# Performance work log

Measured on AMD Instinct MI355X. Metric: run time of the kernel, lower is better.

The kernel has to match this reference:

```python
import jax, jax.numpy as jnp
import numpy as np
from jax.scipy.linalg import expm

B = 524288      # batch of states (original module is per-vector; vmapped via batched matmuls)
IN = 64         # input_size
KDIM = 128      # koopman_size
W_PHI = (IN + KDIM) // 2   # 96, encoder MLP hidden width
W_INV = (KDIM + IN) // 2   # 96, decoder MLP hidden width


def setup_inputs() -> dict:
    key = jax.random.key(0)
    ks = jax.random.split(key, 8)
    def w(k, shape, fan_in):
        return jax.random.normal(k, shape, jnp.float32) / np.float32(np.sqrt(fan_in))
    return {
        "t": jnp.asarray(6.0, jnp.float32),                       # hours; module uses t/24
        "x": jax.random.normal(ks[0], (B, IN), jnp.float32),
        "A": jax.random.normal(ks[1], (KDIM, KDIM), jnp.float32) / np.float32(np.sqrt(KDIM)),
        "phi_W1": w(ks[2], (W_PHI, IN), IN),
        "phi_b1": jnp.zeros((W_PHI,), jnp.float32),
        "phi_W2": w(ks[3], (KDIM, W_PHI), W_PHI),                 # no final bias (skip=True)
        "inv_W1": w(ks[4], (W_INV, KDIM), KDIM),
        "inv_b1": jnp.zeros((W_INV,), jnp.float32),
        "inv_W2": w(ks[5], (IN, W_INV), W_INV),
        "inv_b2": jnp.zeros((IN,), jnp.float32),                  # use_final_bias=True (skip=False)
    }


def reference(t, x, A, phi_W1, phi_b1, phi_W2, inv_W1, inv_b1, inv_W2, inv_b2):
    # phi: z = C @ x + MLP(x), C = eye(KDIM, IN) -> zero-pad x into koopman space
    h = jax.nn.relu(x @ phi_W1.T + phi_b1)                # [B, W_PHI]
    z = jnp.pad(x, ((0, 0), (0, KDIM - IN))) + h @ phi_W2.T   # [B, KDIM]
    # Koopman propagation: K = expm(A * t/24); z <- K @ z (batched as z @ K.T)
    Kmat = expm(A * (t / 24.0), max_squarings=20)          # [KDIM, KDIM]
    z = z @ Kmat.T
    # phi_inv: plain MLP with final bias, no skip
    h2 = jax.nn.relu(z @ inv_W1.T + inv_b1)                # [B, W_INV]
    return h2 @ inv_W2.T + inv_b2                          # [B, IN]
```

## Files before the change

### kernel.cpp

```cpp
#include <hip/hip_runtime.h>

#define BTOT    524288
#define NT64    8192
#define GRID    512
#define TN      6

typedef __attribute__((ext_vector_type(8))) short s8v;
typedef __attribute__((ext_vector_type(4))) float f4v;

#define MFMA(a,b,c) __builtin_amdgcn_mfma_f32_16x16x32_bf16((a),(b),(c),0,0,0)
#define KEEP(x) asm volatile("" : "+v"(x))

__device__ __forceinline__ short f2b(float f) {
  union { float f; unsigned u; } v; v.f = f;
  unsigned r = v.u + 0x7fffu + ((v.u >> 16) & 1u);
  return (short)(r >> 16);
}
__device__ __forceinline__ float b2f(short s) {
  union { float f; unsigned u; } v; v.u = ((unsigned)(unsigned short)s) << 16;
  return v.f;
}
__device__ __forceinline__ s8v pack8(f4v u, f4v v) {
  s8v w;
  w[0] = f2b(u[0]); w[1] = f2b(u[1]); w[2] = f2b(u[2]); w[3] = f2b(u[3]);
  w[4] = f2b(v[0]); w[5] = f2b(v[1]); w[6] = f2b(v[2]); w[7] = f2b(v[3]);
  return w;
}

__device__ __forceinline__ s8v ldfrag(const short* base, int row0, int kbase, int stride) {
  const int l = threadIdx.x & 63;
  return *(const s8v*)(base + (row0 + (l & 15)) * stride + kbase + (l >> 4) * 8);
}

#define WS_M1   0
#define WS_I1   8192
#define WS_W1   20480
#define WS_W2K  26624
#define WS_I2   38912

__device__ __forceinline__ int fragidx(int n, int k, int KS) {
  int jj = n >> 4, ks = k >> 5;
  int l = (n & 15) | (((k >> 3) & 3) << 4);
  return ((jj * KS + ks) * 64 + l) * 8 + (k & 7);
}

__global__ __launch_bounds__(512, 2) void koop_prep(
    const float* __restrict__ tptr, const float* __restrict__ Ag,
    const float* __restrict__ W2g, const float* __restrict__ w1g,
    const float* __restrict__ i1g, const float* __restrict__ i2g,
    short* __restrict__ wsp) {
  extern __shared__ __align__(16) char smem[];
  short* RThi = (short*)smem;
  short* RTlo = RThi + 128 * 136;
  float* sW2  = (float*)(RTlo + 128 * 136);
  float* sred = sW2 + 128 * 96;
  float* scratch = (float*)smem;

  const int tid = threadIdx.x;
  const int lane = tid & 63, wid = tid >> 6;
  const int c_ = lane & 15, g_ = lane >> 4;
  const int mr = wid * 16;

  for (int e = tid; e < 6144; e += 512) {
    wsp[WS_W1 + fragidx(e >> 6, e & 63, 2)] = f2b(w1g[e]);
  }
  for (int e = tid; e < 12288; e += 512) {
    wsp[WS_I1 + fragidx(e >> 7, e & 127, 4)] = f2b(i1g[e]);
  }
  for (int e = tid; e < 6144; e += 512) {
    wsp[WS_I2 + fragidx(e / 96, e % 96, 3)] = f2b(i2g[e]);
  }

  const float s = tptr[0] * (1.0f / 24.0f);
  for (int i = tid; i < 128 * 128; i += 512) scratch[i] = Ag[i] * s;
  for (int i = tid; i < 128 * 96;  i += 512) sW2[i] = W2g[i];
  __syncthreads();

  if (tid < 128) {
    float su = 0.f;
    for (int j = 0; j < 128; ++j) su += fabsf(scratch[tid * 128 + j]);
    sred[tid] = su;
  }
  __syncthreads();
  if (tid == 0) {
    float m = 0.f;
    for (int i = 0; i < 128; ++i) m = fmaxf(m, sred[i]);
    int j = 0; float sc = 1.f;
    while (m > 0.5f && j < 20) { m *= 0.5f; sc *= 0.5f; ++j; }
    sred[128] = (float)j; sred[129] = sc;
  }
  __syncthreads();
  const int jsq = (int)sred[128];
  const float sc = sred[129];

  s8v Ahi[4], Alo[4];
#pragma unroll
  for (int ks = 0; ks < 4; ++ks) {
    const float* p = scratch + (mr + c_) * 128 + ks * 32 + g_ * 8;
    f4v u = *(const f4v*)p, v = *(const f4v*)(p + 4);
    float vals[8] = {u[0], u[1], u[2], u[3], v[0], v[1], v[2], v[3]};
#pragma unroll
    for (int i = 0; i < 8; ++i) {
      float y = vals[i] * sc;
      short h = f2b(y);
      Ahi[ks][i] = h;
      Alo[ks][i] = f2b(y - b2f(h));
    }
  }
  float yv[32];
#pragma unroll
  for (int e = 0; e < 32; ++e) yv[e] = scratch[tid * 32 + e];
  __syncthreads();

#pragma unroll
  for (int e = 0; e < 32; ++e) {
    int idx = tid * 32 + e;
    int r = idx >> 7, c = idx & 127;
    float v = yv[e] * sc * (1.0f / TN) + ((r == c) ? 1.0f : 0.0f);
    short h = f2b(v);
    RThi[c * 136 + r] = h;
    RTlo[c * 136 + r] = f2b(v - b2f(h));
  }
  __syncthreads();

  for (int k = TN - 1; k >= 1; --k) {
    f4v acc[8];
#pragma unroll
    for (int nt = 0; nt < 8; ++nt) acc[nt] = (f4v){0.f, 0.f, 0.f, 0.f};
#pragma unroll
    for (int ks = 0; ks < 4; ++ks) {
#pragma unroll
      for (int nt = 0; nt < 8; ++nt) {
        s8v bh = ldfrag(RThi, nt * 16, ks * 32, 136);
        s8v bl = ldfrag(RTlo, nt * 16, ks * 32, 136);
        acc[nt] = MFMA(Ahi[ks], bh, acc[nt]);
        acc[nt] = MFMA(Alo[ks], bh, acc[nt]);
        acc[nt] = MFMA(Ahi[ks], bl, acc[nt]);
      }
    }
    __syncthreads();
    const float invk = 1.0f / (float)k;
#pragma unroll
    for (int nt = 0; nt < 8; ++nt)
#pragma unroll
      for (int r = 0; r < 4; ++r) {
        int row = mr + g_ * 4 + r, col = nt * 16 + c_;
        float v = acc[nt][r] * invk + ((row == col) ? 1.0f : 0.0f);
        short h = f2b(v);
        RThi[col * 136 + row] = h;
        RTlo[col * 136 + row] = f2b(v - b2f(h));
      }
    __syncthreads();
  }

  for (int it = 0; it < jsq; ++it) {
    s8v Shi[4], Slo[4];
#pragma unroll
    for (int ks = 0; ks < 4; ++ks) {
      int m = mr + c_;
      int k0 = ks * 32 + g_ * 8;
#pragma unroll
      for (int i = 0; i < 8; ++i) {
        Shi[ks][i] = RThi[(k0 + i) * 136 + m];
        Slo[ks][i] = RTlo[(k0 + i) * 136 + m];
      }
    }
    f4v acc[8];
#pragma unroll
    for (int nt = 0; nt < 8; ++nt) acc[nt] = (f4v){0.f, 0.f, 0.f, 0.f};
#pragma unroll
    for (int ks = 0; ks < 4; ++ks) {
#pragma unroll
      for (int nt = 0; nt < 8; ++nt) {
        s8v bh = ldfrag(RThi, nt * 16, ks * 32, 136);
        s8v bl = ldfrag(RTlo, nt * 16, ks * 32, 136);
        acc[nt] = MFMA(Shi[ks], bh, acc[nt]);
        acc[nt] = MFMA(Slo[ks], bh, acc[nt]);
        acc[nt] = MFMA(Shi[ks], bl, acc[nt]);
      }
    }
    __syncthreads();
#pragma unroll
    for (int nt = 0; nt < 8; ++nt)
#pragma unroll
      for (int r = 0; r < 4; ++r) {
        int row = mr + g_ * 4 + r, col = nt * 16 + c_;
        float v = acc[nt][r];
        short h = f2b(v);
        RThi[col * 136 + row] = h;
        RTlo[col * 136 + row] = f2b(v - b2f(h));
      }
    __syncthreads();
  }

  for (int e = tid; e < 128 * 64; e += 512) {
    int n = e >> 6, kk = e & 63;
    float v = b2f(RThi[kk * 136 + n]) + b2f(RTlo[kk * 136 + n]);
    wsp[WS_M1 + fragidx(n, kk, 2)] = f2b(v);
  }

  {
    s8v Shi[4], Slo[4];
#pragma unroll
    for (int ks = 0; ks < 4; ++ks) {
      int m = mr + c_;
      int k0 = ks * 32 + g_ * 8;
#pragma unroll
      for (int i = 0; i < 8; ++i) {
        Shi[ks][i] = RThi[(k0 + i) * 136 + m];
        Slo[ks][i] = RTlo[(k0 + i) * 136 + m];
      }
    }
    f4v acc[6];
#pragma unroll
    for (int nt = 0; nt < 6; ++nt) acc[nt] = (f4v){0.f, 0.f, 0.f, 0.f};
#pragma unroll
    for (int ks = 0; ks < 4; ++ks) {
#pragma unroll
      for (int nt = 0; nt < 6; ++nt) {
        s8v bh, bl;
#pragma unroll
        for (int i = 0; i < 8; ++i) {
          float v = sW2[(ks * 32 + g_ * 8 + i) * 96 + nt * 16 + c_];
          short h = f2b(v);
          bh[i] = h;
          bl[i] = f2b(v - b2f(h));
        }
        acc[nt] = MFMA(Shi[ks], bh, acc[nt]);
        acc[nt] = MFMA(Slo[ks], bh, acc[nt]);
        acc[nt] = MFMA(Shi[ks], bl, acc[nt]);
      }
    }
#pragma unroll
    for (int nt = 0; nt < 6; ++nt)
#pragma unroll
      for (int r = 0; r < 4; ++r)
        wsp[WS_W2K + fragidx(mr + g_ * 4 + r, nt * 16 + c_, 3)] = f2b(acc[nt][r]);
  }
}

__global__ __launch_bounds__(256, 2) void koop_main(
    const float* __restrict__ xg, const float* __restrict__ b1g,
    const float* __restrict__ bi1g, const float* __restrict__ bi2g,
    const short* __restrict__ wsp, float* __restrict__ outg) {
  extern __shared__ __align__(16) char smem[];
  short* sM1 = (short*)smem;
  short* sI1 = sM1 + 8192;
  short* sX  = sI1 + 12288;
  short* sH  = sX + 4096;
  short* sZ  = sH + 6144;

  const int tid = threadIdx.x;
  const int lane = tid & 63, wid = tid >> 6;
  const int c_ = lane & 15, g_ = lane >> 4;
  const int rg = wid >> 1, cg = wid & 1;

  for (int i = tid; i < (8192 + 12288) / 8; i += 256)
    ((f4v*)sM1)[i] = ((const f4v*)(wsp + WS_M1))[i];

  f4v wW1[3][2], wW2K[4][3], wI2[2][3];
  float bH[3], bH2[3], bO[2];
#pragma unroll
  for (int j = 0; j < 3; ++j) {
    bH[j]  = b1g[(cg * 3 + j) * 16 + c_];
    bH2[j] = bi1g[(cg * 3 + j) * 16 + c_];
#pragma unroll
    for (int ks = 0; ks < 2; ++ks) {
      wW1[j][ks] = *(const f4v*)(wsp + WS_W1 + (((cg * 3 + j) * 2 + ks) * 64 + lane) * 8);
      KEEP(wW1[j][ks]);
    }
  }
#pragma unroll
  for (int j = 0; j < 4; ++j)
#pragma unroll
    for (int ks = 0; ks < 3; ++ks) {
      wW2K[j][ks] = *(const f4v*)(wsp + WS_W2K + (((cg * 4 + j) * 3 + ks) * 64 + lane) * 8);
      KEEP(wW2K[j][ks]);
    }
#pragma unroll
  for (int j = 0; j < 2; ++j) {
    bO[j] = bi2g[(cg * 2 + j) * 16 + c_];
#pragma unroll
    for (int ks = 0; ks < 3; ++ks) {
      wI2[j][ks] = *(const f4v*)(wsp + WS_I2 + (((cg * 2 + j) * 3 + ks) * 64 + lane) * 8);
      KEEP(wI2[j][ks]);
    }
  }

  const int s0 = tid, s1 = tid + 256;
  int srow[2], sk0[2];
#pragma unroll
  for (int q = 0; q < 2; ++q) {
    int s = q ? s1 : s0;
    int cid = s >> 6, sl = s & 63;
    srow[q] = (cid >> 2) * 32 + ((cid >> 1) & 1) * 16 + (sl & 15);
    sk0[q]  = (cid & 1) * 32 + (sl >> 4) * 8;
  }

  int tile = blockIdx.x;
  {
    const float* p0 = xg + ((size_t)tile * 64 + srow[0]) * 64 + sk0[0];
    const float* p1 = xg + ((size_t)tile * 64 + srow[1]) * 64 + sk0[1];
    *(s8v*)(sX + s0 * 8) = pack8(*(const f4v*)p0, *(const f4v*)(p0 + 4));
    *(s8v*)(sX + s1 * 8) = pack8(*(const f4v*)p1, *(const f4v*)(p1 + 4));
  }
  __syncthreads();

  for (; tile < NT64; tile += GRID) {
    const int nxt = tile + GRID;
    f4v pv0, pv1, pv2, pv3;
    if (nxt < NT64) {
      const float* p0 = xg + ((size_t)nxt * 64 + srow[0]) * 64 + sk0[0];
      const float* p1 = xg + ((size_t)nxt * 64 + srow[1]) * 64 + sk0[1];
      pv0 = *(const f4v*)p0; pv1 = *(const f4v*)(p0 + 4);
      pv2 = *(const f4v*)p1; pv3 = *(const f4v*)(p1 + 4);
    }

    s8v ax[2][2];
#pragma unroll
    for (int mi = 0; mi < 2; ++mi) {
#pragma unroll
      for (int ks = 0; ks < 2; ++ks)
        ax[mi][ks] = *(const s8v*)(sX + (((rg * 2 + mi) * 2 + ks) * 64 + lane) * 8);
#pragma unroll
      for (int j = 0; j < 3; ++j) {
        f4v acc = (f4v){bH[j], bH[j], bH[j], bH[j]};
        acc = MFMA(ax[mi][0], __builtin_bit_cast(s8v, wW1[j][0]), acc);
        acc = MFMA(ax[mi][1], __builtin_bit_cast(s8v, wW1[j][1]), acc);
        const int cb = (cg * 3 + j) * 16;
        const int ks3 = cb >> 5, hb = ((cb >> 3) & 3) + (c_ >> 3);
#pragma unroll
        for (int r = 0; r < 4; ++r) {
          float v = acc[r]; v = v > 0.f ? v : 0.f;
          sH[(((rg * 2 + mi) * 3 + ks3) * 64 + ((g_ * 4 + r) | (hb << 4))) * 8 + (c_ & 7)] = f2b(v);
        }
      }
    }
    __syncthreads();

    if (nxt < NT64) {
      *(s8v*)(sX + s0 * 8) = pack8(pv0, pv1);
      *(s8v*)(sX + s1 * 8) = pack8(pv2, pv3);
    }

#pragma unroll
    for (int mi = 0; mi < 2; ++mi) {
      s8v ah0 = *(const s8v*)(sH + (((rg * 2 + mi) * 3 + 0) * 64 + lane) * 8);
      s8v ah1 = *(const s8v*)(sH + (((rg * 2 + mi) * 3 + 1) * 64 + lane) * 8);
      s8v ah2 = *(const s8v*)(sH + (((rg * 2 + mi) * 3 + 2) * 64 + lane) * 8);
#pragma unroll
      for (int j = 0; j < 4; ++j) {
        s8v m0 = *(const s8v*)(sM1 + (((cg * 4 + j) * 2 + 0) * 64 + lane) * 8);
        s8v m1 = *(const s8v*)(sM1 + (((cg * 4 + j) * 2 + 1) * 64 + lane) * 8);
        f4v acc = (f4v){0.f, 0.f, 0.f, 0.f};
        acc = MFMA(ax[mi][0], m0, acc);
        acc = MFMA(ax[mi][1], m1, acc);
        acc = MFMA(ah0, __builtin_bit_cast(s8v, wW2K[j][0]), acc);
        acc = MFMA(ah1, __builtin_bit_cast(s8v, wW2K[j][1]), acc);
        acc = MFMA(ah2, __builtin_bit_cast(s8v, wW2K[j][2]), acc);
        const int cb = (cg * 4 + j) * 16;
        const int ks4 = cb >> 5, hb = ((cb >> 3) & 3) + (c_ >> 3);
#pragma unroll
        for (int r = 0; r < 4; ++r)
          sZ[(((rg * 2 + mi) * 4 + ks4) * 64 + ((g_ * 4 + r) | (hb << 4))) * 8 + (c_ & 7)] = f2b(acc[r]);
      }
    }
    __syncthreads();

#pragma unroll
    for (int mi = 0; mi < 2; ++mi) {
      s8v az[4];
#pragma unroll
      for (int ks = 0; ks < 4; ++ks)
        az[ks] = *(const s8v*)(sZ + (((rg * 2 + mi) * 4 + ks) * 64 + lane) * 8);
#pragma unroll
      for (int j = 0; j < 3; ++j) {
        f4v acc = (f4v){bH2[j], bH2[j], bH2[j], bH2[j]};
#pragma unroll
        for (int ks = 0; ks < 4; ++ks) {
          s8v bfrag = *(const s8v*)(sI1 + (((cg * 3 + j) * 4 + ks) * 64 + lane) * 8);
          acc = MFMA(az[ks], bfrag, acc);
        }
        const int cb = (cg * 3 + j) * 16;
        const int ks3 = cb >> 5, hb = ((cb >> 3) & 3) + (c_ >> 3);
#pragma unroll
        for (int r = 0; r < 4; ++r) {
          float v = acc[r]; v = v > 0.f ? v : 0.f;
          sH[(((rg * 2 + mi) * 3 + ks3) * 64 + ((g_ * 4 + r) | (hb << 4))) * 8 + (c_ & 7)] = f2b(v);
        }
      }
    }
    __syncthreads();

#pragma unroll
    for (int mi = 0; mi < 2; ++mi) {
      s8v a0 = *(const s8v*)(sH + (((rg * 2 + mi) * 3 + 0) * 64 + lane) * 8);
      s8v a1 = *(const s8v*)(sH + (((rg * 2 + mi) * 3 + 1) * 64 + lane) * 8);
      s8v a2 = *(const s8v*)(sH + (((rg * 2 + mi) * 3 + 2) * 64 + lane) * 8);
#pragma unroll
      for (int j = 0; j < 2; ++j) {
        f4v acc = (f4v){bO[j], bO[j], bO[j], bO[j]};
        acc = MFMA(a0, __builtin_bit_cast(s8v, wI2[j][0]), acc);
        acc = MFMA(a1, __builtin_bit_cast(s8v, wI2[j][1]), acc);
        acc = MFMA(a2, __builtin_bit_cast(s8v, wI2[j][2]), acc);
#pragma unroll
        for (int r = 0; r < 4; ++r)
          outg[((size_t)tile * 64 + rg * 32 + mi * 16 + g_ * 4 + r) * 64 +
               (cg * 2 + j) * 16 + c_] = acc[r];
      }
    }
    __syncthreads();
  }
}

#define PREP_LDS (128 * 136 * 2 * 2 + 128 * 96 * 4 + 130 * 4)
#define MAIN_LDS ((8192 + 12288 + 4096 + 6144 + 8192) * 2)

extern "C" void kernel_launch(void* const* d_in, const int* in_sizes, int n_in,
                              void* d_out, int out_size, void* d_ws, size_t ws_size,
                              hipStream_t stream) {
  (void)in_sizes; (void)n_in; (void)out_size; (void)ws_size;
  const float* t     = (const float*)d_in[0];
  const float* x     = (const float*)d_in[1];
  const float* A     = (const float*)d_in[2];
  const float* phiW1 = (const float*)d_in[3];
  const float* phib1 = (const float*)d_in[4];
  const float* phiW2 = (const float*)d_in[5];
  const float* invW1 = (const float*)d_in[6];
  const float* invb1 = (const float*)d_in[7];
  const float* invW2 = (const float*)d_in[8];
  const float* invb2 = (const float*)d_in[9];
  float* out = (float*)d_out;
  short* wsp = (short*)d_ws;

  (void)hipFuncSetAttribute((const void*)koop_prep,
                            hipFuncAttributeMaxDynamicSharedMemorySize, PREP_LDS);
  (void)hipFuncSetAttribute((const void*)koop_main,
                            hipFuncAttributeMaxDynamicSharedMemorySize, MAIN_LDS);

  koop_prep<<<1, 512, PREP_LDS, stream>>>(t, A, phiW2, phiW1, invW1, invW2, wsp);
  koop_main<<<GRID, 256, MAIN_LDS, stream>>>(x, phib1, invb1, invb2, wsp, out);
}
```

Baseline: 144.2 us.

## Swap MFMA operand roles so activations are B operand with padded row-major LDS

The main kernel now computes the transposed products: weights become the A operand and batch activations the B operand. Each lane's accumulator then holds four consecutive feature values, so the bf16 results go to padded row-major LDS buffers as single 8-byte stores, and the final output goes out as 16-byte float4 stores instead of scalar scattered writes. The x staging becomes a simple row-major load, and the M1/I1 fragments are hoisted into registers before each batch loop. Risks include different LDS bank conflict patterns from the padding strides and higher register pressure from the hoisted fragments.

```diff
diff --git a/kernel.cpp b/kernel.cpp
--- a/kernel.cpp
+++ b/kernel.cpp
@@ -5,7 +5,12 @@
 #define GRID    512
 #define TN      6
 
+#define SX 72
+#define SH 104
+#define SZ 136
+
 typedef __attribute__((ext_vector_type(8))) short s8v;
+typedef __attribute__((ext_vector_type(4))) short s4v;
 typedef __attribute__((ext_vector_type(4))) float f4v;
 
 #define MFMA(a,b,c) __builtin_amdgcn_mfma_f32_16x16x32_bf16((a),(b),(c),0,0,0)
@@ -26,10 +31,24 @@
   w[4] = f2b(v[0]); w[5] = f2b(v[1]); w[6] = f2b(v[2]); w[7] = f2b(v[3]);
   return w;
 }
+__device__ __forceinline__ s4v pack4(f4v a) {
+  s4v w; w[0]=f2b(a[0]); w[1]=f2b(a[1]); w[2]=f2b(a[2]); w[3]=f2b(a[3]); return w;
+}
+__device__ __forceinline__ s4v pack4r(f4v a) {
+  s4v w;
+  w[0]=f2b(fmaxf(a[0],0.f)); w[1]=f2b(fmaxf(a[1],0.f));
+  w[2]=f2b(fmaxf(a[2],0.f)); w[3]=f2b(fmaxf(a[3],0.f));
+  return w;
+}
 
 __device__ __forceinline__ s8v ldfrag(const short* base, int row0, int kbase, int stride) {
   const int l = threadIdx.x & 63;
   return *(const s8v*)(base + (row0 + (l & 15)) * stride + kbase + (l >> 4) * 8);
+}
+
+__device__ __forceinline__ s8v ldact(const short* base, int col0, int kbase, int stride) {
+  const int l = threadIdx.x & 63;
+  return *(const s8v*)(base + (col0 + (l & 15)) * stride + kbase + (l >> 4) * 8);
 }
 
 #define WS_M1   0
@@ -61,15 +80,12 @@
   const int c_ = lane & 15, g_ = lane >> 4;
   const int mr = wid * 16;
 
-  for (int e = tid; e < 6144; e += 512) {
+  for (int e = tid; e < 6144; e += 512)
     wsp[WS_W1 + fragidx(e >> 6, e & 63, 2)] = f2b(w1g[e]);
-  }
-  for (int e = tid; e < 12288; e += 512) {
+  for (int e = tid; e < 12288; e += 512)
     wsp[WS_I1 + fragidx(e >> 7, e & 127, 4)] = f2b(i1g[e]);
-  }
-  for (int e = tid; e < 6144; e += 512) {
+  for (int e = tid; e < 6144; e += 512)
     wsp[WS_I2 + fragidx(e / 96, e % 96, 3)] = f2b(i2g[e]);
-  }
 
   const float s = tptr[0] * (1.0f / 24.0f);
   for (int i = tid; i < 128 * 128; i += 512) scratch[i] = Ag[i] * s;
@@ -244,65 +260,56 @@
     const float* __restrict__ bi1g, const float* __restrict__ bi2g,
     const short* __restrict__ wsp, float* __restrict__ outg) {
   extern __shared__ __align__(16) char smem[];
-  short* sM1 = (short*)smem;
-  short* sI1 = sM1 + 8192;
-  short* sX  = sI1 + 12288;
-  short* sH  = sX + 4096;
-  short* sZ  = sH + 6144;
+  short* sM1f = (short*)smem;
+  short* sI1f = sM1f + 8192;
+  short* sX   = sI1f + 12288;
+  short* sH   = sX + 64 * SX;
+  short* sZ   = sH + 64 * SH;
 
   const int tid = threadIdx.x;
   const int lane = tid & 63, wid = tid >> 6;
   const int c_ = lane & 15, g_ = lane >> 4;
-  const int rg = wid >> 1, cg = wid & 1;
-
-  for (int i = tid; i < (8192 + 12288) / 8; i += 256)
-    ((f4v*)sM1)[i] = ((const f4v*)(wsp + WS_M1))[i];
+  const int bg = wid >> 1, fg = wid & 1;
+
+  for (int i = tid; i < 20480 / 8; i += 256)
+    ((f4v*)sM1f)[i] = ((const f4v*)(wsp + WS_M1))[i];
 
   f4v wW1[3][2], wW2K[4][3], wI2[2][3];
-  float bH[3], bH2[3], bO[2];
-#pragma unroll
-  for (int j = 0; j < 3; ++j) {
-    bH[j]  = b1g[(cg * 3 + j) * 16 + c_];
-    bH2[j] = bi1g[(cg * 3 + j) * 16 + c_];
+  f4v bW1[3], bI1[3], bI2[2];
+#pragma unroll
+  for (int fb = 0; fb < 3; ++fb) {
+    bW1[fb] = *(const f4v*)(b1g  + (fg * 3 + fb) * 16 + g_ * 4);  KEEP(bW1[fb]);
+    bI1[fb] = *(const f4v*)(bi1g + (fg * 3 + fb) * 16 + g_ * 4);  KEEP(bI1[fb]);
 #pragma unroll
     for (int ks = 0; ks < 2; ++ks) {
-      wW1[j][ks] = *(const f4v*)(wsp + WS_W1 + (((cg * 3 + j) * 2 + ks) * 64 + lane) * 8);
-      KEEP(wW1[j][ks]);
-    }
-  }
-#pragma unroll
-  for (int j = 0; j < 4; ++j)
+      wW1[fb][ks] = *(const f4v*)(wsp + WS_W1 + (((fg * 3 + fb) * 2 + ks) * 64 + lane) * 8);
+      KEEP(wW1[fb][ks]);
+    }
+  }
+#pragma unroll
+  for (int fb = 0; fb < 4; ++fb)
 #pragma unroll
     for (int ks = 0; ks < 3; ++ks) {
-      wW2K[j][ks] = *(const f4v*)(wsp + WS_W2K + (((cg * 4 + j) * 3 + ks) * 64 + lane) * 8);
-      KEEP(wW2K[j][ks]);
-    }
-#pragma unroll
-  for (int j = 0; j < 2; ++j) {
-    bO[j] = bi2g[(cg * 2 + j) * 16 + c_];
+      wW2K[fb][ks] = *(const f4v*)(wsp + WS_W2K + (((fg * 4 + fb) * 3 + ks) * 64 + lane) * 8);
+      KEEP(wW2K[fb][ks]);
+    }
+#pragma unroll
+  for (int fb = 0; fb < 2; ++fb) {
+    bI2[fb] = *(const f4v*)(bi2g + (fg * 2 + fb) * 16 + g_ * 4);  KEEP(bI2[fb]);
 #pragma unroll
     for (int ks = 0; ks < 3; ++ks) {
-      wI2[j][ks] = *(const f4v*)(wsp + WS_I2 + (((cg * 2 + j) * 3 + ks) * 64 + lane) * 8);
-      KEEP(wI2[j][ks]);
-    }
-  }
-
-  const int s0 = tid, s1 = tid + 256;
-  int srow[2], sk0[2];
-#pragma unroll
-  for (int q = 0; q < 2; ++q) {
-    int s = q ? s1 : s0;
-    int cid = s >> 6, sl = s & 63;
-    srow[q] = (cid >> 2) * 32 + ((cid >> 1) & 1) * 16 + (sl & 15);
-    sk0[q]  = (cid & 1) * 32 + (sl >> 4) * 8;
-  }
+      wI2[fb][ks] = *(const f4v*)(wsp + WS_I2 + (((fg * 2 + fb) * 3 + ks) * 64 + lane) * 8);
+      KEEP(wI2[fb][ks]);
+    }
+  }
+
+  const int xr = tid >> 2, xq = tid & 3;
 
   int tile = blockIdx.x;
   {
-    const float* p0 = xg + ((size_t)tile * 64 + srow[0]) * 64 + sk0[0];
-    const float* p1 = xg + ((size_t)tile * 64 + srow[1]) * 64 + sk0[1];
-    *(s8v*)(sX + s0 * 8) = pack8(*(const f4v*)p0, *(const f4v*)(p0 + 4));
-    *(s8v*)(sX + s1 * 8) = pack8(*(const f4v*)p1, *(const f4v*)(p1 + 4));
+    const float* src = xg + ((size_t)tile * 64 + xr) * 64 + xq * 16;
+    *(s8v*)(sX + xr * SX + xq * 16) = pack8(*(const f4v*)src, *(const f4v*)(src + 4));
+    *(s8v*)(sX + xr * SX + xq * 16 + 8) = pack8(*(const f4v*)(src + 8), *(const f4v*)(src + 12));
   }
   __syncthreads();
 
@@ -310,103 +317,92 @@
     const int nxt = tile + GRID;
     f4v pv0, pv1, pv2, pv3;
     if (nxt < NT64) {
-      const float* p0 = xg + ((size_t)nxt * 64 + srow[0]) * 64 + sk0[0];
-      const float* p1 = xg + ((size_t)nxt * 64 + srow[1]) * 64 + sk0[1];
-      pv0 = *(const f4v*)p0; pv1 = *(const f4v*)(p0 + 4);
-      pv2 = *(const f4v*)p1; pv3 = *(const f4v*)(p1 + 4);
-    }
-
-    s8v ax[2][2];
-#pragma unroll
-    for (int mi = 0; mi < 2; ++mi) {
+      const float* src = xg + ((size_t)nxt * 64 + xr) * 64 + xq * 16;
+      pv0 = *(const f4v*)src;       pv1 = *(const f4v*)(src + 4);
+      pv2 = *(const f4v*)(src + 8); pv3 = *(const f4v*)(src + 12);
+    }
+
+    s8v bx[2][2];
+#pragma unroll
+    for (int bb = 0; bb < 2; ++bb) {
+      const int col0 = (bg * 2 + bb) * 16;
+      bx[bb][0] = ldact(sX, col0, 0, SX);
+      bx[bb][1] = ldact(sX, col0, 32, SX);
+#pragma unroll
+      for (int fb = 0; fb < 3; ++fb) {
+        f4v acc = bW1[fb];
+        acc = MFMA(__builtin_bit_cast(s8v, wW1[fb][0]), bx[bb][0], acc);
+        acc = MFMA(__builtin_bit_cast(s8v, wW1[fb][1]), bx[bb][1], acc);
+        *(s4v*)(sH + (col0 + c_) * SH + (fg * 3 + fb) * 16 + g_ * 4) = pack4r(acc);
+      }
+    }
+    __syncthreads();
+
+    if (nxt < NT64) {
+      *(s8v*)(sX + xr * SX + xq * 16) = pack8(pv0, pv1);
+      *(s8v*)(sX + xr * SX + xq * 16 + 8) = pack8(pv2, pv3);
+    }
+
+    s8v m1f[4][2];
+#pragma unroll
+    for (int fb = 0; fb < 4; ++fb)
 #pragma unroll
       for (int ks = 0; ks < 2; ++ks)
-        ax[mi][ks] = *(const s8v*)(sX + (((rg * 2 + mi) * 2 + ks) * 64 + lane) * 8);
-#pragma unroll
-      for (int j = 0; j < 3; ++j) {
-        f4v acc = (f4v){bH[j], bH[j], bH[j], bH[j]};
-        acc = MFMA(ax[mi][0], __builtin_bit_cast(s8v, wW1[j][0]), acc);
-        acc = MFMA(ax[mi][1], __builtin_bit_cast(s8v, wW1[j][1]), acc);
-        const int cb = (cg * 3 + j) * 16;
-        const int ks3 = cb >> 5, hb = ((cb >> 3) & 3) + (c_ >> 3);
-#pragma unroll
-        for (int r = 0; r < 4; ++r) {
-          float v = acc[r]; v = v > 0.f ? v : 0.f;
-          sH[(((rg * 2 + mi) * 3 + ks3) * 64 + ((g_ * 4 + r) | (hb << 4))) * 8 + (c_ & 7)] = f2b(v);
-        }
-      }
-    }
-    __syncthreads();
-
-    if (nxt < NT64) {
-      *(s8v*)(sX + s0 * 8) = pack8(pv0, pv1);
-      *(s8v*)(sX + s1 * 8) = pack8(pv2, pv3);
-    }
-
-#pragma unroll
-    for (int mi = 0; mi < 2; ++mi) {
-      s8v ah0 = *(const s8v*)(sH + (((rg * 2 + mi) * 3 + 0) * 64 + lane) * 8);
-      s8v ah1 = *(const s8v*)(sH + (((rg * 2 + mi) * 3 + 1) * 64 + lane) * 8);
-      s8v ah2 = *(const s8v*)(sH + (((rg * 2 + mi) * 3 + 2) * 64 + lane) * 8);
-#pragma unroll
-      for (int j = 0; j < 4; ++j) {
-        s8v m0 = *(const s8v*)(sM1 + (((cg * 4 + j) * 2 + 0) * 64 + lane) * 8);
-        s8v m1 = *(const s8v*)(sM1 + (((cg * 4 + j) * 2 + 1) * 64 + lane) * 8);
+        m1f[fb][ks] = *(const s8v*)(sM1f + (((fg * 4 + fb) * 2 + ks) * 64 + lane) * 8);
+#pragma unroll
+    for (int bb = 0; bb < 2; ++bb) {
+      const int col0 = (bg * 2 + bb) * 16;
+      s8v hb0 = ldact(sH, col0, 0, SH);
+      s8v hb1 = ldact(sH, col0, 32, SH);
+      s8v hb2 = ldact(sH, col0, 64, SH);
+#pragma unroll
+      for (int fb = 0; fb < 4; ++fb) {
         f4v acc = (f4v){0.f, 0.f, 0.f, 0.f};
-        acc = MFMA(ax[mi][0], m0, acc);
-        acc = MFMA(ax[mi][1], m1, acc);
-        acc = MFMA(ah0, __builtin_bit_cast(s8v, wW2K[j][0]), acc);
-        acc = MFMA(ah1, __builtin_bit_cast(s8v, wW2K[j][1]), acc);
-        acc = MFMA(ah2, __builtin_bit_cast(s8v, wW2K[j][2]), acc);
-        const int cb = (cg * 4 + j) * 16;
-        const int ks4 = cb >> 5, hb = ((cb >> 3) & 3) + (c_ >> 3);
-#pragma unroll
-        for (int r = 0; r < 4; ++r)
-          sZ[(((rg * 2 + mi) * 4 + ks4) * 64 + ((g_ * 4 + r) | (hb << 4))) * 8 + (c_ & 7)] = f2b(acc[r]);
-      }
-    }
-    __syncthreads();
-
-#pragma unroll
-    for (int mi = 0; mi < 2; ++mi) {
-      s8v az[4];
+        acc = MFMA(m1f[fb][0], bx[bb][0], acc);
+        acc = MFMA(m1f[fb][1], bx[bb][1], acc);
+        acc = MFMA(__builtin_bit_cast(s8v, wW2K[fb][0]), hb0, acc);
+        acc = MFMA(__builtin_bit_cast(s8v, wW2K[fb][1]), hb1, acc);
+        acc = MFMA(__builtin_bit_cast(s8v, wW2K[fb][2]), hb2, acc);
+        *(s4v*)(sZ + (col0 + c_) * SZ + (fg * 4 + fb) * 16 + g_ * 4) = pack4(acc);
+      }
+    }
+    __syncthreads();
+
+    s8v i1f[3][4];
+#pragma unroll
+    for (int fb = 0; fb < 3; ++fb)
 #pragma unroll
       for (int ks = 0; ks < 4; ++ks)
-        az[ks] = *(const s8v*)(sZ + (((rg * 2 + mi) * 4 + ks) * 64 + lane) * 8);
-#pragma unroll
-      for (int j = 0; j < 3; ++j) {
-        f4v acc = (f4v){bH2[j], bH2[j], bH2[j], bH2[j]};
-#pragma unroll
-        for (int ks = 0; ks < 4; ++ks) {
-          s8v bfrag = *(const s8v*)(sI1 + (((cg * 3 + j) * 4 + ks) * 64 + lane) * 8);
-          acc = MFMA(az[ks], bfrag, acc);
-        }
-        const int cb = (cg * 3 + j) * 16;
-        const int ks3 = cb >> 5, hb = ((cb >> 3) & 3) + (c_ >> 3);
-#pragma unroll
-        for (int r = 0; r < 4; ++r) {
-          float v = acc[r]; v = v > 0.f ? v : 0.f;
-          sH[(((rg * 2 + mi) * 3 + ks3) * 64 + ((g_ * 4 + r) | (hb << 4))) * 8 + (c_ & 7)] = f2b(v);
-        }
-      }
-    }
-    __syncthreads();
-
-#pragma unroll
-    for (int mi = 0; mi < 2; ++mi) {
-      s8v a0 = *(const s8v*)(sH + (((rg * 2 + mi) * 3 + 0) * 64 + lane) * 8);
-      s8v a1 = *(const s8v*)(sH + (((rg * 2 + mi) * 3 + 1) * 64 + lane) * 8);
-      s8v a2 = *(const s8v*)(sH + (((rg * 2 + mi) * 3 + 2) * 64 + lane) * 8);
-#pragma unroll
-      for (int j = 0; j < 2; ++j) {
-        f4v acc = (f4v){bO[j], bO[j], bO[j], bO[j]};
-        acc = MFMA(a0, __builtin_bit_cast(s8v, wI2[j][0]), acc);
-        acc = MFMA(a1, __builtin_bit_cast(s8v, wI2[j][1]), acc);
-        acc = MFMA(a2, __builtin_bit_cast(s8v, wI2[j][2]), acc);
-#pragma unroll
-        for (int r = 0; r < 4; ++r)
-          outg[((size_t)tile * 64 + rg * 32 + mi * 16 + g_ * 4 + r) * 64 +
-               (cg * 2 + j) * 16 + c_] = acc[r];
+        i1f[fb][ks] = *(const s8v*)(sI1f + (((fg * 3 + fb) * 4 + ks) * 64 + lane) * 8);
+#pragma unroll
+    for (int bb = 0; bb < 2; ++bb) {
+      const int col0 = (bg * 2 + bb) * 16;
+      s8v zb[4];
+#pragma unroll
+      for (int ks = 0; ks < 4; ++ks) zb[ks] = ldact(sZ, col0, ks * 32, SZ);
+#pragma unroll
+      for (int fb = 0; fb < 3; ++fb) {
+        f4v acc = bI1[fb];
+#pragma unroll
+        for (int ks = 0; ks < 4; ++ks) acc = MFMA(i1f[fb][ks], zb[ks], acc);
+        *(s4v*)(sH + (col0 + c_) * SH + (fg * 3 + fb) * 16 + g_ * 4) = pack4r(acc);
+      }
+    }
+    __syncthreads();
+
+#pragma unroll
+    for (int bb = 0; bb < 2; ++bb) {
+      const int col0 = (bg * 2 + bb) * 16;
+      s8v h0 = ldact(sH, col0, 0, SH);
+      s8v h1 = ldact(sH, col0, 32, SH);
+      s8v h2 = ldact(sH, col0, 64, SH);
+#pragma unroll
+      for (int fb = 0; fb < 2; ++fb) {
+        f4v acc = bI2[fb];
+        acc = MFMA(__builtin_bit_cast(s8v, wI2[fb][0]), h0, acc);
+        acc = MFMA(__builtin_bit_cast(s8v, wI2[fb][1]), h1, acc);
+        acc = MFMA(__builtin_bit_cast(s8v, wI2[fb][2]), h2, acc);
+        *(f4v*)(outg + ((size_t)tile * 64 + col0 + c_) * 64 + (fg * 2 + fb) * 16 + g_ * 4) = acc;
       }
     }
     __syncthreads();
@@ -414,7 +410,7 @@
 }
 
 #define PREP_LDS (128 * 136 * 2 * 2 + 128 * 96 * 4 + 130 * 4)
-#define MAIN_LDS ((8192 + 12288 + 4096 + 6144 + 8192) * 2)
+#define MAIN_LDS ((8192 + 12288 + 64 * SX + 64 * SH + 64 * SZ) * 2)
 
 extern "C" void kernel_launch(void* const* d_in, const int* in_sizes, int n_in,
                               void* d_out, int out_size, void* d_ws, size_t ws_size,
```

Measured after the change: 139.6 us. -3.2%, faster.
